# Kernel tuning notes

Measured on AMD Instinct MI355X. Metric: run time of the kernel, lower is better.

Reference implementation:

```python
import jax, jax.numpy as jnp
import numpy as np

B, S, H = 4, 2048, 1024   # batch, seq, hidden
D = 2048                  # expert intermediate (SwiGLU MLP)
E = 8                     # n_routed_experts
K = 2                     # num_experts_per_tok


def setup_inputs() -> dict:
    key = jax.random.key(0)
    ks = jax.random.split(key, 8)
    w = lambda k, shape: (jax.random.normal(k, shape, jnp.float32) * 0.02)
    return {
        "hidden_states": jax.random.normal(ks[0], (B, S, H), jnp.float32),
        "gate_w": w(ks[1], (H, E)),       # router logits projection
        "w_gate": w(ks[2], (E, H, D)),    # routed experts: gate_proj
        "w_up":   w(ks[3], (E, H, D)),    # routed experts: up_proj
        "w_down": w(ks[4], (E, D, H)),    # routed experts: down_proj
        "ws_gate": w(ks[5], (H, D)),      # shared expert: gate_proj
        "ws_up":   w(ks[6], (H, D)),      # shared expert: up_proj
        "ws_down": w(ks[7], (D, H)),      # shared expert: down_proj
    }


def reference(hidden_states, gate_w, w_gate, w_up, w_down, ws_gate, ws_up, ws_down):
    b, s, h = hidden_states.shape
    x = hidden_states.reshape(-1, h)                      # [N, H], N = B*S

    # --- MoeGate: softmax over experts, top-k, renormalize top-k weights ---
    scores = jax.nn.softmax(x @ gate_w, axis=-1)          # [N, E]
    topk_w, topk_idx = jax.lax.top_k(scores, K)           # [N, K]
    topk_w = topk_w / (jnp.sum(topk_w, axis=-1, keepdims=True) + 1e-20)

    # Combine per-token top-k weights into a dense per-expert weight [N, E].
    # Equivalent to the sort-based dispatch + index_add combine in the original:
    # each token's output is sum_k topk_w[n,k] * expert_{topk_idx[n,k]}(x[n]).
    onehot = jax.nn.one_hot(topk_idx, E, dtype=x.dtype)   # [N, K, E]
    w_per_expert = jnp.einsum('nke,nk->ne', onehot, topk_w)  # [N, E]

    # --- routed experts (SwiGLU MLP), fixed small loop over experts ---
    y = jnp.zeros_like(x)
    for e in range(E):
        hid = jax.nn.silu(x @ w_gate[e]) * (x @ w_up[e])  # [N, D]
        y = y + w_per_expert[:, e:e + 1] * (hid @ w_down[e])

    # --- shared expert applied to all tokens ---
    shared = (jax.nn.silu(x @ ws_gate) * (x @ ws_up)) @ ws_down
    return (y + shared).reshape(b, s, h)
```

## Files before the change

### kernel.cpp

```cpp
#include <hip/hip_runtime.h>
#include <hip/hip_bf16.h>
#include <stdint.h>

#define N_TOK 8192
#define H_DIM 1024
#define D_DIM 2048
#define NEXP  8

#define NSLOT      16384
#define SHARED_ROW 16512
#define HID_ROWS   24704

typedef __attribute__((ext_vector_type(8))) short          bf16x8;
typedef __attribute__((ext_vector_type(4))) float          f32x4;
typedef __attribute__((ext_vector_type(8))) unsigned short u16x8;

__device__ __forceinline__ unsigned short f2bf(float f) {
    union { float f; uint32_t u; } v; v.f = f;
    uint32_t r = v.u + 0x7fff + ((v.u >> 16) & 1);
    return (unsigned short)(r >> 16);
}

__device__ __forceinline__ void gll16(const void* g, void* l) {
    __builtin_amdgcn_global_load_lds(
        (const __attribute__((address_space(1))) void*)g,
        (__attribute__((address_space(3))) void*)l, 16, 0, 0);
}

__global__ void k_router(const float* __restrict__ x, const float* __restrict__ gw,
                         int* __restrict__ tok_e, float* __restrict__ tok_w,
                         int* __restrict__ counts) {
    int l = threadIdx.x & 63;
    int n = blockIdx.x * 4 + (threadIdx.x >> 6);
    const float* xr = x + (size_t)n * H_DIM + l * 16;
    float acc[NEXP];
#pragma unroll
    for (int e = 0; e < NEXP; ++e) acc[e] = 0.f;
#pragma unroll
    for (int j = 0; j < 16; ++j) {
        float xv = xr[j];
        const float4* g4 = (const float4*)(gw + (size_t)(l * 16 + j) * NEXP);
        float4 g0 = g4[0], g1 = g4[1];
        acc[0] += xv * g0.x; acc[1] += xv * g0.y; acc[2] += xv * g0.z; acc[3] += xv * g0.w;
        acc[4] += xv * g1.x; acc[5] += xv * g1.y; acc[6] += xv * g1.z; acc[7] += xv * g1.w;
    }
#pragma unroll
    for (int off = 32; off >= 1; off >>= 1) {
#pragma unroll
        for (int e = 0; e < NEXP; ++e) acc[e] += __shfl_xor(acc[e], off);
    }
    if (l == 0) {
        int e0 = 0; float v0 = acc[0];
#pragma unroll
        for (int e = 1; e < NEXP; ++e) if (acc[e] > v0) { v0 = acc[e]; e0 = e; }
        int e1 = -1; float v1 = -1e30f;
#pragma unroll
        for (int e = 0; e < NEXP; ++e) if (e != e0 && acc[e] > v1) { v1 = acc[e]; e1 = e; }
        float t  = expf(v1 - v0);
        float w1 = t / (1.f + t);
        float w0 = 1.f - w1;
        tok_e[2 * n]     = e0;  tok_e[2 * n + 1] = e1;
        tok_w[2 * n]     = w0;  tok_w[2 * n + 1] = w1;
        atomicAdd(&counts[e0], 1);
        atomicAdd(&counts[e1], 1);
    }
}

__global__ void k_scan(const int* __restrict__ counts, int* __restrict__ offs) {
    if (threadIdx.x == 0) {
        int s = 0;
        for (int e = 0; e < NEXP; ++e) { offs[e] = s; s += counts[e]; }
    }
}

__global__ void k_assign(const int* __restrict__ tok_e, const float* __restrict__ tok_w,
                         const int* __restrict__ offs, int* __restrict__ cursor,
                         int* __restrict__ slot_token, float* __restrict__ slot_weight) {
    int n = blockIdx.x * 256 + threadIdx.x;
#pragma unroll
    for (int k = 0; k < 2; ++k) {
        int e   = tok_e[2 * n + k];
        float w = tok_w[2 * n + k];
        int pos = atomicAdd(&cursor[e], 1);
        int s   = offs[e] + pos;
        slot_token[s]  = n;
        slot_weight[s] = w;
    }
}

__global__ void k_cvt_x(const float* __restrict__ x, unsigned short* __restrict__ xb) {
    size_t i = ((size_t)blockIdx.x * 256 + threadIdx.x) * 8;
    float4 a = *(const float4*)(x + i);
    float4 b = *(const float4*)(x + i + 4);
    u16x8 o;
    o[0] = f2bf(a.x); o[1] = f2bf(a.y); o[2] = f2bf(a.z); o[3] = f2bf(a.w);
    o[4] = f2bf(b.x); o[5] = f2bf(b.y); o[6] = f2bf(b.z); o[7] = f2bf(b.w);
    *(u16x8*)(xb + i) = o;
}

__global__ void k_tconv(const float* __restrict__ src, unsigned short* __restrict__ dst,
                        int R, int C) {
    __shared__ float tb[64][65];
    size_t mb = (size_t)blockIdx.z * (size_t)R * C;
    src += mb; dst += mb;
    int t = threadIdx.x;
    int r0 = blockIdx.y * 64, c0 = blockIdx.x * 64;
    int c4 = t & 15, rr = t >> 4;
#pragma unroll
    for (int p = 0; p < 4; ++p) {
        int r = p * 16 + rr;
        float4 v = *(const float4*)(src + (size_t)(r0 + r) * C + c0 + c4 * 4);
        tb[r][c4 * 4 + 0] = v.x; tb[r][c4 * 4 + 1] = v.y;
        tb[r][c4 * 4 + 2] = v.z; tb[r][c4 * 4 + 3] = v.w;
    }
    __syncthreads();
    int rbase = (t & 7) * 8;
#pragma unroll
    for (int p = 0; p < 2; ++p) {
        int cc = p * 32 + (t >> 3);
        u16x8 o;
#pragma unroll
        for (int j = 0; j < 8; ++j) o[j] = f2bf(tb[rbase + j][cc]);
        *(u16x8*)(dst + (size_t)(c0 + cc) * R + r0 + rbase) = o;
    }
}

__global__ __launch_bounds__(256, 3) void k_gemm1(
    const unsigned short* __restrict__ xb,
    const unsigned short* __restrict__ wg_t, const unsigned short* __restrict__ wu_t,
    const unsigned short* __restrict__ wsg_t, const unsigned short* __restrict__ wsu_t,
    const int* __restrict__ counts, const int* __restrict__ offs,
    const int* __restrict__ slot_token, unsigned short* __restrict__ hid) {
    int g = blockIdx.z;
    int n_g, sbase, hbase;
    if (g < NEXP) { n_g = counts[g]; sbase = offs[g]; hbase = sbase; }
    else          { n_g = N_TOK;     sbase = 0;       hbase = SHARED_ROW; }
    int rt = blockIdx.y;
    if (rt * 128 >= n_g) return;
    int dt = blockIdx.x;

    const unsigned short* Bg = (g < NEXP) ? wg_t + (size_t)g * D_DIM * H_DIM : wsg_t;
    const unsigned short* Bu = (g < NEXP) ? wu_t + (size_t)g * D_DIM * H_DIM : wsu_t;

    __shared__ __attribute__((aligned(16))) char smem[32 * 1024];
    char* sA  = smem;
    char* sBg = smem + 16384;
    char* sBu = smem + 24576;

    int t = threadIdx.x;
    int w = t >> 6, l = t & 63;
    int lr8 = l >> 3, lc8 = l & 7;
    int swz = ((lc8 ^ lr8) << 4);

    const char* aptr[4]; char* ldsa[4];
#pragma unroll
    for (int c = 0; c < 4; ++c) {
        int chunk = w * 4 + c;
        int row = chunk * 8 + lr8;
        int r = rt * 128 + row;
        int tk;
        if (g == NEXP) tk = r;
        else           tk = (r < n_g) ? slot_token[sbase + r] : slot_token[sbase];
        aptr[c] = (const char*)xb + ((size_t)tk * H_DIM) * 2 + swz;
        ldsa[c] = sA + chunk * 1024;
    }
    const char* bgptr[2]; const char* buptr[2]; char* ldsbg[2]; char* ldsbu[2];
#pragma unroll
    for (int c = 0; c < 2; ++c) {
        int chunk = w * 2 + c;
        int row = chunk * 8 + lr8;
        int nn = dt * 64 + row;
        bgptr[c] = (const char*)Bg + ((size_t)nn * H_DIM) * 2 + swz;
        buptr[c] = (const char*)Bu + ((size_t)nn * H_DIM) * 2 + swz;
        ldsbg[c] = sBg + chunk * 1024;
        ldsbu[c] = sBu + chunk * 1024;
    }

    f32x4 accg[4][2], accu[4][2];
#pragma unroll
    for (int m = 0; m < 4; ++m)
#pragma unroll
        for (int n = 0; n < 2; ++n) { accg[m][n] = 0.f; accu[m][n] = 0.f; }

    int wr = w >> 1, wc = w & 1;
    int lr = l & 15, lg = l >> 4;
    int rsw = (lr & 7) << 4;

    for (int ks = 0; ks < H_DIM / 64; ++ks) {
        int kb = ks * 128;
#pragma unroll
        for (int c = 0; c < 4; ++c) gll16(aptr[c] + kb, ldsa[c]);
#pragma unroll
        for (int c = 0; c < 2; ++c) {
            gll16(bgptr[c] + kb, ldsbg[c]);
            gll16(buptr[c] + kb, ldsbu[c]);
        }
        __syncthreads();
#pragma unroll
        for (int ksub = 0; ksub < 2; ++ksub) {
            int c0 = (ksub * 64 + lg * 16) ^ rsw;
            bf16x8 a[4], bg[2], bu[2];
#pragma unroll
            for (int m = 0; m < 4; ++m)
                a[m] = *(const bf16x8*)(sA + (wr * 64 + m * 16 + lr) * 128 + c0);
#pragma unroll
            for (int n = 0; n < 2; ++n) {
                bg[n] = *(const bf16x8*)(sBg + (wc * 32 + n * 16 + lr) * 128 + c0);
                bu[n] = *(const bf16x8*)(sBu + (wc * 32 + n * 16 + lr) * 128 + c0);
            }
#pragma unroll
            for (int m = 0; m < 4; ++m)
#pragma unroll
                for (int n = 0; n < 2; ++n) {
                    accg[m][n] = __builtin_amdgcn_mfma_f32_16x16x32_bf16(a[m], bg[n], accg[m][n], 0, 0, 0);
                    accu[m][n] = __builtin_amdgcn_mfma_f32_16x16x32_bf16(a[m], bu[n], accu[m][n], 0, 0, 0);
                }
        }
        __syncthreads();
    }

    int cb = dt * 64 + wc * 32;
#pragma unroll
    for (int m = 0; m < 4; ++m)
#pragma unroll
        for (int n = 0; n < 2; ++n)
#pragma unroll
            for (int i = 0; i < 4; ++i) {
                int row = rt * 128 + wr * 64 + m * 16 + lg * 4 + i;
                if (row < n_g) {
                    float gv = accg[m][n][i], uv = accu[m][n][i];
                    float hv = (gv / (1.f + __expf(-gv))) * uv;
                    int col = cb + n * 16 + lr;
                    hid[(size_t)(hbase + row) * D_DIM + col] = f2bf(hv);
                }
            }
}

template <int MODE>
__global__ __launch_bounds__(256, 3) void k_gemm2(
    const unsigned short* __restrict__ hid,
    const unsigned short* __restrict__ wd_t, const unsigned short* __restrict__ wsd_t,
    const int* __restrict__ counts, const int* __restrict__ offs,
    const int* __restrict__ slot_token, const float* __restrict__ slot_weight,
    float* __restrict__ out) {
    int n_g, abase;
    const unsigned short* B;
    if (MODE == 0) { n_g = N_TOK; abase = SHARED_ROW; B = wsd_t; }
    else {
        int g = blockIdx.z;
        n_g = counts[g]; abase = offs[g];
        B = wd_t + (size_t)g * H_DIM * D_DIM;
    }
    int rt = blockIdx.y;
    if (rt * 128 >= n_g) return;
    int ct = blockIdx.x;

    __shared__ __attribute__((aligned(16))) char smem[32 * 1024];
    __shared__ int   sTok[128];
    __shared__ float sW[128];
    char* sA = smem; char* sB = smem + 16384;

    int t = threadIdx.x, w = t >> 6, l = t & 63;
    if (MODE == 1 && t < 128) {
        int r = rt * 128 + t;
        sTok[t] = (r < n_g) ? slot_token[abase + r]  : 0;
        sW[t]   = (r < n_g) ? slot_weight[abase + r] : 0.f;
    }
    int lr8 = l >> 3, lc8 = l & 7;
    int swz = ((lc8 ^ lr8) << 4);
    const char* aptr[4]; const char* bptr[4];
    char* ldsa[4]; char* ldsb[4];
#pragma unroll
    for (int c = 0; c < 4; ++c) {
        int chunk = w * 4 + c;
        int row = chunk * 8 + lr8;
        aptr[c] = (const char*)hid + ((size_t)(abase + rt * 128 + row) * D_DIM) * 2 + swz;
        int nn  = ct * 128 + row;
        bptr[c] = (const char*)B + ((size_t)nn * D_DIM) * 2 + swz;
        ldsa[c] = sA + chunk * 1024;
        ldsb[c] = sB + chunk * 1024;
    }
    f32x4 acc[4][4];
#pragma unroll
    for (int m = 0; m < 4; ++m)
#pragma unroll
        for (int n = 0; n < 4; ++n) acc[m][n] = 0.f;

    int wr = w >> 1, wc = w & 1, lr = l & 15, lg = l >> 4;
    int rsw = (lr & 7) << 4;

    for (int ks = 0; ks < D_DIM / 64; ++ks) {
        int kb = ks * 128;
#pragma unroll
        for (int c = 0; c < 4; ++c) {
            gll16(aptr[c] + kb, ldsa[c]);
            gll16(bptr[c] + kb, ldsb[c]);
        }
        __syncthreads();
#pragma unroll
        for (int ksub = 0; ksub < 2; ++ksub) {
            int c0 = (ksub * 64 + lg * 16) ^ rsw;
            bf16x8 a[4], b[4];
#pragma unroll
            for (int m = 0; m < 4; ++m)
                a[m] = *(const bf16x8*)(sA + (wr * 64 + m * 16 + lr) * 128 + c0);
#pragma unroll
            for (int n = 0; n < 4; ++n)
                b[n] = *(const bf16x8*)(sB + (wc * 64 + n * 16 + lr) * 128 + c0);
#pragma unroll
            for (int m = 0; m < 4; ++m)
#pragma unroll
                for (int n = 0; n < 4; ++n)
                    acc[m][n] = __builtin_amdgcn_mfma_f32_16x16x32_bf16(a[m], b[n], acc[m][n], 0, 0, 0);
        }
        __syncthreads();
    }

    int cb = ct * 128 + wc * 64;
#pragma unroll
    for (int m = 0; m < 4; ++m)
#pragma unroll
        for (int n = 0; n < 4; ++n)
#pragma unroll
            for (int i = 0; i < 4; ++i) {
                int tr = wr * 64 + m * 16 + lg * 4 + i;
                int col = cb + n * 16 + lr;
                if (MODE == 0) {
                    out[(size_t)(rt * 128 + tr) * H_DIM + col] = acc[m][n][i];
                } else {
                    if (rt * 128 + tr < n_g) {
                        int tok = sTok[tr]; float wgt = sW[tr];
                        unsafeAtomicAdd(&out[(size_t)tok * H_DIM + col], acc[m][n][i] * wgt);
                    }
                }
            }
}

extern "C" void kernel_launch(void* const* d_in, const int* in_sizes, int n_in,
                              void* d_out, int out_size, void* d_ws, size_t ws_size,
                              hipStream_t stream) {
    const float* x       = (const float*)d_in[0];
    const float* gw      = (const float*)d_in[1];
    const float* w_gate  = (const float*)d_in[2];
    const float* w_up    = (const float*)d_in[3];
    const float* w_down  = (const float*)d_in[4];
    const float* ws_gate = (const float*)d_in[5];
    const float* ws_up   = (const float*)d_in[6];
    const float* ws_down = (const float*)d_in[7];
    float* out = (float*)d_out;
    char* ws = (char*)d_ws;

    const size_t oXB    = 0;
    const size_t oWG    = oXB    + (size_t)N_TOK * H_DIM * 2;
    const size_t oWU    = oWG    + (size_t)NEXP * D_DIM * H_DIM * 2;
    const size_t oWD    = oWU    + (size_t)NEXP * D_DIM * H_DIM * 2;
    const size_t oWSG   = oWD    + (size_t)NEXP * H_DIM * D_DIM * 2;
    const size_t oWSU   = oWSG   + (size_t)D_DIM * H_DIM * 2;
    const size_t oWSD   = oWSU   + (size_t)D_DIM * H_DIM * 2;
    const size_t oHID   = oWSD   + (size_t)H_DIM * D_DIM * 2;
    const size_t oTOKE  = oHID   + (size_t)HID_ROWS * D_DIM * 2;
    const size_t oTOKW  = oTOKE  + (size_t)N_TOK * 2 * 4;
    const size_t oSLOTT = oTOKW  + (size_t)N_TOK * 2 * 4;
    const size_t oSLOTW = oSLOTT + (size_t)(NSLOT + 128) * 4;
    const size_t oCTRL  = oSLOTW + (size_t)(NSLOT + 128) * 4;

    unsigned short* xb    = (unsigned short*)(ws + oXB);
    unsigned short* wg_t  = (unsigned short*)(ws + oWG);
    unsigned short* wu_t  = (unsigned short*)(ws + oWU);
    unsigned short* wd_t  = (unsigned short*)(ws + oWD);
    unsigned short* wsg_t = (unsigned short*)(ws + oWSG);
    unsigned short* wsu_t = (unsigned short*)(ws + oWSU);
    unsigned short* wsd_t = (unsigned short*)(ws + oWSD);
    unsigned short* hid   = (unsigned short*)(ws + oHID);
    int*   tok_e       = (int*)(ws + oTOKE);
    float* tok_w       = (float*)(ws + oTOKW);
    int*   slot_token  = (int*)(ws + oSLOTT);
    float* slot_weight = (float*)(ws + oSLOTW);
    int*   counts      = (int*)(ws + oCTRL);
    int*   offs        = counts + 8;
    int*   cursor      = counts + 16;

    hipMemsetAsync(counts, 0, 256, stream);
    k_router<<<N_TOK / 4, 256, 0, stream>>>(x, gw, tok_e, tok_w, counts);
    k_scan<<<1, 64, 0, stream>>>(counts, offs);
    k_assign<<<N_TOK / 256, 256, 0, stream>>>(tok_e, tok_w, offs, cursor, slot_token, slot_weight);

    k_cvt_x<<<(N_TOK * H_DIM) / (8 * 256), 256, 0, stream>>>(x, xb);
    k_tconv<<<dim3(D_DIM / 64, H_DIM / 64, NEXP), 256, 0, stream>>>(w_gate, wg_t, H_DIM, D_DIM);
    k_tconv<<<dim3(D_DIM / 64, H_DIM / 64, NEXP), 256, 0, stream>>>(w_up,   wu_t, H_DIM, D_DIM);
    k_tconv<<<dim3(H_DIM / 64, D_DIM / 64, NEXP), 256, 0, stream>>>(w_down, wd_t, D_DIM, H_DIM);
    k_tconv<<<dim3(D_DIM / 64, H_DIM / 64, 1),    256, 0, stream>>>(ws_gate, wsg_t, H_DIM, D_DIM);
    k_tconv<<<dim3(D_DIM / 64, H_DIM / 64, 1),    256, 0, stream>>>(ws_up,   wsu_t, H_DIM, D_DIM);
    k_tconv<<<dim3(H_DIM / 64, D_DIM / 64, 1),    256, 0, stream>>>(ws_down, wsd_t, D_DIM, H_DIM);

    k_gemm1<<<dim3(32, 64, NEXP + 1), 256, 0, stream>>>(xb, wg_t, wu_t, wsg_t, wsu_t,
                                                        counts, offs, slot_token, hid);
    k_gemm2<0><<<dim3(8, 64, 1), 256, 0, stream>>>(hid, wd_t, wsd_t, counts, offs,
                                                   slot_token, slot_weight, out);
    k_gemm2<1><<<dim3(8, 64, NEXP), 256, 0, stream>>>(hid, wd_t, wsd_t, counts, offs,
                                                      slot_token, slot_weight, out);
}
```

Measured before the change: 929.0 us.

## Fold routing weight into gemm1 epilogue and shrink gemm2 N-tile to 64

Moves the per-slot routing weight multiplication from the gemm2 atomic epilogue into gemm1, so the bf16 hidden activations are pre-scaled. gemm2 now uses a 128x64 output tile instead of 128x128, doubling the grid and halving B-tile loads and accumulators. Both kernels ask for occupancy 4 instead of 3. The smaller tile lowers register and LDS pressure and adds parallelism, at the cost of reading the A tile twice as often; scaling before the bf16 rounding slightly changes numerics.

```diff
diff --git a/kernel.cpp b/kernel.cpp
--- a/kernel.cpp
+++ b/kernel.cpp
@@ -125,12 +125,13 @@
     }
 }
 
-__global__ __launch_bounds__(256, 3) void k_gemm1(
+__global__ __launch_bounds__(256, 4) void k_gemm1(
     const unsigned short* __restrict__ xb,
     const unsigned short* __restrict__ wg_t, const unsigned short* __restrict__ wu_t,
     const unsigned short* __restrict__ wsg_t, const unsigned short* __restrict__ wsu_t,
     const int* __restrict__ counts, const int* __restrict__ offs,
-    const int* __restrict__ slot_token, unsigned short* __restrict__ hid) {
+    const int* __restrict__ slot_token, const float* __restrict__ slot_weight,
+    unsigned short* __restrict__ hid) {
     int g = blockIdx.z;
     int n_g, sbase, hbase;
     if (g < NEXP) { n_g = counts[g]; sbase = offs[g]; hbase = sbase; }
@@ -143,12 +144,17 @@
     const unsigned short* Bu = (g < NEXP) ? wu_t + (size_t)g * D_DIM * H_DIM : wsu_t;
 
     __shared__ __attribute__((aligned(16))) char smem[32 * 1024];
+    __shared__ float sWt[128];
     char* sA  = smem;
     char* sBg = smem + 16384;
     char* sBu = smem + 24576;
 
     int t = threadIdx.x;
     int w = t >> 6, l = t & 63;
+    if (t < 128) {
+        int r = rt * 128 + t;
+        sWt[t] = (g < NEXP) ? ((r < n_g) ? slot_weight[sbase + r] : 0.f) : 1.f;
+    }
     int lr8 = l >> 3, lc8 = l & 7;
     int swz = ((lc8 ^ lr8) << 4);
 
@@ -226,10 +232,11 @@
         for (int n = 0; n < 2; ++n)
 #pragma unroll
             for (int i = 0; i < 4; ++i) {
-                int row = rt * 128 + wr * 64 + m * 16 + lg * 4 + i;
+                int trow = wr * 64 + m * 16 + lg * 4 + i;
+                int row = rt * 128 + trow;
                 if (row < n_g) {
                     float gv = accg[m][n][i], uv = accu[m][n][i];
-                    float hv = (gv / (1.f + __expf(-gv))) * uv;
+                    float hv = (gv / (1.f + __expf(-gv))) * uv * sWt[trow];
                     int col = cb + n * 16 + lr;
                     hid[(size_t)(hbase + row) * D_DIM + col] = f2bf(hv);
                 }
@@ -237,12 +244,11 @@
 }
 
 template <int MODE>
-__global__ __launch_bounds__(256, 3) void k_gemm2(
+__global__ __launch_bounds__(256, 4) void k_gemm2(
     const unsigned short* __restrict__ hid,
     const unsigned short* __restrict__ wd_t, const unsigned short* __restrict__ wsd_t,
     const int* __restrict__ counts, const int* __restrict__ offs,
-    const int* __restrict__ slot_token, const float* __restrict__ slot_weight,
-    float* __restrict__ out) {
+    const int* __restrict__ slot_token, float* __restrict__ out) {
     int n_g, abase;
     const unsigned short* B;
     if (MODE == 0) { n_g = N_TOK; abase = SHARED_ROW; B = wsd_t; }
@@ -255,36 +261,39 @@
     if (rt * 128 >= n_g) return;
     int ct = blockIdx.x;
 
-    __shared__ __attribute__((aligned(16))) char smem[32 * 1024];
-    __shared__ int   sTok[128];
-    __shared__ float sW[128];
-    char* sA = smem; char* sB = smem + 16384;
+    __shared__ __attribute__((aligned(16))) char smem[24 * 1024];
+    __shared__ int sTok[128];
+    char* sA = smem;
+    char* sB = smem + 16384;
 
     int t = threadIdx.x, w = t >> 6, l = t & 63;
     if (MODE == 1 && t < 128) {
         int r = rt * 128 + t;
-        sTok[t] = (r < n_g) ? slot_token[abase + r]  : 0;
-        sW[t]   = (r < n_g) ? slot_weight[abase + r] : 0.f;
+        sTok[t] = (r < n_g) ? slot_token[abase + r] : 0;
     }
     int lr8 = l >> 3, lc8 = l & 7;
     int swz = ((lc8 ^ lr8) << 4);
-    const char* aptr[4]; const char* bptr[4];
-    char* ldsa[4]; char* ldsb[4];
+    const char* aptr[4]; char* ldsa[4];
 #pragma unroll
     for (int c = 0; c < 4; ++c) {
         int chunk = w * 4 + c;
         int row = chunk * 8 + lr8;
         aptr[c] = (const char*)hid + ((size_t)(abase + rt * 128 + row) * D_DIM) * 2 + swz;
-        int nn  = ct * 128 + row;
-        bptr[c] = (const char*)B + ((size_t)nn * D_DIM) * 2 + swz;
         ldsa[c] = sA + chunk * 1024;
+    }
+    const char* bptr[2]; char* ldsb[2];
+#pragma unroll
+    for (int c = 0; c < 2; ++c) {
+        int chunk = w * 2 + c;
+        int row = chunk * 8 + lr8;
+        bptr[c] = (const char*)B + ((size_t)(ct * 64 + row) * D_DIM) * 2 + swz;
         ldsb[c] = sB + chunk * 1024;
     }
-    f32x4 acc[4][4];
+    f32x4 acc[4][2];
 #pragma unroll
     for (int m = 0; m < 4; ++m)
 #pragma unroll
-        for (int n = 0; n < 4; ++n) acc[m][n] = 0.f;
+        for (int n = 0; n < 2; ++n) acc[m][n] = 0.f;
 
     int wr = w >> 1, wc = w & 1, lr = l & 15, lg = l >> 4;
     int rsw = (lr & 7) << 4;
@@ -292,35 +301,34 @@
     for (int ks = 0; ks < D_DIM / 64; ++ks) {
         int kb = ks * 128;
 #pragma unroll
-        for (int c = 0; c < 4; ++c) {
-            gll16(aptr[c] + kb, ldsa[c]);
-            gll16(bptr[c] + kb, ldsb[c]);
-        }
+        for (int c = 0; c < 4; ++c) gll16(aptr[c] + kb, ldsa[c]);
+#pragma unroll
+        for (int c = 0; c < 2; ++c) gll16(bptr[c] + kb, ldsb[c]);
         __syncthreads();
 #pragma unroll
         for (int ksub = 0; ksub < 2; ++ksub) {
             int c0 = (ksub * 64 + lg * 16) ^ rsw;
-            bf16x8 a[4], b[4];
+            bf16x8 a[4], b[2];
 #pragma unroll
             for (int m = 0; m < 4; ++m)
                 a[m] = *(const bf16x8*)(sA + (wr * 64 + m * 16 + lr) * 128 + c0);
 #pragma unroll
-            for (int n = 0; n < 4; ++n)
-                b[n] = *(const bf16x8*)(sB + (wc * 64 + n * 16 + lr) * 128 + c0);
+            for (int n = 0; n < 2; ++n)
+                b[n] = *(const bf16x8*)(sB + (wc * 32 + n * 16 + lr) * 128 + c0);
 #pragma unroll
             for (int m = 0; m < 4; ++m)
 #pragma unroll
-                for (int n = 0; n < 4; ++n)
+                for (int n = 0; n < 2; ++n)
                     acc[m][n] = __builtin_amdgcn_mfma_f32_16x16x32_bf16(a[m], b[n], acc[m][n], 0, 0, 0);
         }
         __syncthreads();
     }
 
-    int cb = ct * 128 + wc * 64;
+    int cb = ct * 64 + wc * 32;
 #pragma unroll
     for (int m = 0; m < 4; ++m)
 #pragma unroll
-        for (int n = 0; n < 4; ++n)
+        for (int n = 0; n < 2; ++n)
 #pragma unroll
             for (int i = 0; i < 4; ++i) {
                 int tr = wr * 64 + m * 16 + lg * 4 + i;
@@ -329,8 +337,8 @@
                     out[(size_t)(rt * 128 + tr) * H_DIM + col] = acc[m][n][i];
                 } else {
                     if (rt * 128 + tr < n_g) {
-                        int tok = sTok[tr]; float wgt = sW[tr];
-                        unsafeAtomicAdd(&out[(size_t)tok * H_DIM + col], acc[m][n][i] * wgt);
+                        int tok = sTok[tr];
+                        unsafeAtomicAdd(&out[(size_t)tok * H_DIM + col], acc[m][n][i]);
                     }
                 }
             }
@@ -394,9 +402,9 @@
     k_tconv<<<dim3(H_DIM / 64, D_DIM / 64, 1),    256, 0, stream>>>(ws_down, wsd_t, D_DIM, H_DIM);
 
     k_gemm1<<<dim3(32, 64, NEXP + 1), 256, 0, stream>>>(xb, wg_t, wu_t, wsg_t, wsu_t,
-                                                        counts, offs, slot_token, hid);
-    k_gemm2<0><<<dim3(8, 64, 1), 256, 0, stream>>>(hid, wd_t, wsd_t, counts, offs,
-                                                   slot_token, slot_weight, out);
-    k_gemm2<1><<<dim3(8, 64, NEXP), 256, 0, stream>>>(hid, wd_t, wsd_t, counts, offs,
-                                                      slot_token, slot_weight, out);
-}
+                                                        counts, offs, slot_token, slot_weight, hid);
+    k_gemm2<0><<<dim3(16, 64, 1), 256, 0, stream>>>(hid, wd_t, wsd_t, counts, offs,
+                                                    slot_token, out);
+    k_gemm2<1><<<dim3(16, 64, NEXP), 256, 0, stream>>>(hid, wd_t, wsd_t, counts, offs,
+                                                       slot_token, out);
+}
```

After: 936.4 us. About the same (+0.8%).
